# Kernel optimization log

Hardware: AMD Instinct MI355X
Metric: run time of the kernel (lower is better)

Reference implementation:

```python
import jax, jax.numpy as jnp
import numpy as np

N = 50000      # num nodes
E = 800000     # num edges (avg degree 16)
IN_FEA = 256
OU_FEA = 64


def setup_inputs() -> dict:
    key = jax.random.key(0)
    k_h, k_w, k_r, k_c, k_v = jax.random.split(key, 5)
    h = jax.random.normal(k_h, (N, IN_FEA), dtype=jnp.float32)
    # Linear(in_fea, ou_fea, bias=None): weight applied as h @ W, W [IN, OUT]
    W = jax.random.normal(k_w, (IN_FEA, OU_FEA), dtype=jnp.float32) / np.sqrt(IN_FEA)
    row = jax.random.randint(k_r, (E,), 0, N, dtype=jnp.int32)
    col = jax.random.randint(k_c, (E,), 0, N, dtype=jnp.int32)
    vals = jax.random.uniform(k_v, (E,), dtype=jnp.float32)
    return {"h": h, "W": W, "row": row, "col": col, "vals": vals}


def reference(h, W, row, col, vals):
    # dense projection: [N, IN] @ [IN, OUT] -> [N, OUT]
    hp = h @ W
    # torch builds sparse tensor with indices [col, row], i.e. G = A^T,
    # so torch.sparse.mm(G, hp)[i] = sum over edges with col==i of vals * hp[row]
    msg = hp[row] * vals[:, None]                      # [E, OUT] gather + scale
    out = jax.ops.segment_sum(msg, col, num_segments=N)  # scatter-add to dest
    return out
```

## Files before the change

### kernel.cpp

```cpp
#include <hip/hip_runtime.h>
#include <hip/hip_bf16.h>

#define IN_F 256
#define OU_F 64
#define BKN 128
#define BSHIFT 7
#define NBMAX 512
#define CHUNK 4096
#define STAGE_CAP 4096

typedef __attribute__((ext_vector_type(8))) short short8;
typedef __attribute__((ext_vector_type(4))) float f32x4;

__global__ void __launch_bounds__(256)
gemm_mfma_kernel(const float* __restrict__ h, const float* __restrict__ W,
                 __hip_bfloat16* __restrict__ hp, int* __restrict__ bcnt, int N)
{
    __shared__ unsigned short Wt[64][264];
    __shared__ uint4 hsv[2048];
    unsigned char* hs = reinterpret_cast<unsigned char*>(hsv);
    const int t = threadIdx.x;

    if (blockIdx.x == 0)
        for (int i = t; i <= NBMAX; i += 256) bcnt[i] = 0;

#pragma unroll
    for (int i = 0; i < 32; ++i) {
        int p  = t + i * 256;
        int c  = p & 63;
        int k0 = (p >> 6) << 1;
        float x = W[(size_t)k0 * OU_F + c];
        float y = W[(size_t)(k0 + 1) * OU_F + c];
        __hip_bfloat162 bb = __float22bfloat162_rn(make_float2(x, y));
        *reinterpret_cast<unsigned*>(&Wt[c][k0]) = *reinterpret_cast<unsigned*>(&bb);
    }

    const int rbase = blockIdx.x * 64;
    const int nrow  = min(64, N - rbase);
#pragma unroll
    for (int i = 0; i < 16; ++i) {
        int idx = t + i * 256;
        int r  = idx >> 6;
        int k4 = idx & 63;
        float4 v = make_float4(0.f, 0.f, 0.f, 0.f);
        if (r < nrow)
            v = reinterpret_cast<const float4*>(h)[(size_t)(rbase + r) * (IN_F / 4) + k4];
        __hip_bfloat162 lo = __float22bfloat162_rn(make_float2(v.x, v.y));
        __hip_bfloat162 hi = __float22bfloat162_rn(make_float2(v.z, v.w));
        unsigned boff = (unsigned)r * 512u + (((unsigned)k4 * 8u) ^ (((unsigned)r & 7u) << 4));
        uint2 pk;
        pk.x = *reinterpret_cast<unsigned*>(&lo);
        pk.y = *reinterpret_cast<unsigned*>(&hi);
        *reinterpret_cast<uint2*>(&hs[boff]) = pk;
    }
    __syncthreads();

    const int l    = t & 63;
    const int wv   = t >> 6;
    const int cl   = l & 15;
    const int kg   = l >> 4;
    const int rloc = wv * 16 + cl;

    f32x4 acc[4];
#pragma unroll
    for (int nt = 0; nt < 4; ++nt) acc[nt] = (f32x4){0.f, 0.f, 0.f, 0.f};

#pragma unroll
    for (int ks = 0; ks < 8; ++ks) {
        unsigned aoff = (unsigned)rloc * 512u +
                        (((unsigned)(ks * 64 + kg * 16)) ^ (((unsigned)rloc & 7u) << 4));
        short8 af = *reinterpret_cast<const short8*>(&hs[aoff]);
#pragma unroll
        for (int nt = 0; nt < 4; ++nt) {
            short8 bf = *reinterpret_cast<const short8*>(&Wt[nt * 16 + cl][ks * 32 + kg * 8]);
            acc[nt] = __builtin_amdgcn_mfma_f32_16x16x32_bf16(af, bf, acc[nt], 0, 0, 0);
        }
    }

#pragma unroll
    for (int nt = 0; nt < 4; ++nt)
#pragma unroll
        for (int rg = 0; rg < 4; ++rg) {
            int rr = rbase + wv * 16 + kg * 4 + rg;
            if (rr < N)
                hp[(size_t)rr * OU_F + nt * 16 + cl] = __float2bfloat16(acc[nt][rg]);
        }
}

__global__ void __launch_bounds__(256)
hist_scan_kernel(const int* __restrict__ col, int* __restrict__ bcnt,
                 int* __restrict__ boffs, int* __restrict__ bcursor, int E, int NB)
{
    __shared__ int lh[NBMAX];
    __shared__ int s[256];
    __shared__ int isLast;
    const int t = threadIdx.x;

    for (int i = t; i < NB; i += 256) lh[i] = 0;
    __syncthreads();

    const int n4 = E >> 2;
    const int4* c4 = (const int4*)col;
    for (int i = blockIdx.x * 256 + t; i < n4; i += gridDim.x * 256) {
        int4 v = c4[i];
        atomicAdd(&lh[v.x >> BSHIFT], 1);
        atomicAdd(&lh[v.y >> BSHIFT], 1);
        atomicAdd(&lh[v.z >> BSHIFT], 1);
        atomicAdd(&lh[v.w >> BSHIFT], 1);
    }
    if (blockIdx.x == 0)
        for (int e = (n4 << 2) + t; e < E; e += 256)
            atomicAdd(&lh[col[e] >> BSHIFT], 1);
    __syncthreads();

    for (int i = t; i < NB; i += 256)
        if (lh[i]) atomicAdd(&bcnt[i], lh[i]);

    __threadfence();
    if (t == 0) {
        int v = atomicAdd(&bcnt[NBMAX], 1);
        isLast = (v == (int)gridDim.x - 1);
    }
    __syncthreads();
    if (!isLast) return;

    for (int i = t; i < NB; i += 256)
        lh[i] = __hip_atomic_load(&bcnt[i], __ATOMIC_RELAXED, __HIP_MEMORY_SCOPE_AGENT);
    __syncthreads();

    int idx = t * 2;
    int c0 = (idx     < NB) ? lh[idx]     : 0;
    int c1 = (idx + 1 < NB) ? lh[idx + 1] : 0;
    int s0 = c0, s1 = s0 + c1;
    s[t] = s1;
    __syncthreads();
    for (int d = 1; d < 256; d <<= 1) {
        int v = (t >= d) ? s[t - d] : 0;
        __syncthreads();
        s[t] += v;
        __syncthreads();
    }
    int excl = (t > 0) ? s[t - 1] : 0;
    if (idx     < NB) { boffs[idx]     = excl;      bcursor[idx]     = excl;      }
    if (idx + 1 < NB) { boffs[idx + 1] = excl + s0; bcursor[idx + 1] = excl + s0; }
    if (t == 255) boffs[NB] = s[255];
}

__global__ void __launch_bounds__(256)
partition_kernel(const int* __restrict__ row, const int* __restrict__ col,
                 const float* __restrict__ vals, int* __restrict__ bcursor,
                 int2* __restrict__ epk, int E, int NB)
{
    __shared__ int  hist[NBMAX];
    __shared__ int  X[NBMAX];
    __shared__ int  gshift[NBMAX];
    __shared__ int  s[256];
    __shared__ int2 stage[CHUNK];
    __shared__ int  gpos[CHUNK];

    const int t = threadIdx.x;
    const int base = blockIdx.x * CHUNK;
    const int n = min(CHUNK, E - base);

    for (int i = t; i < NBMAX; i += 256) hist[i] = 0;
    __syncthreads();

#pragma unroll
    for (int k = 0; k < CHUNK / 256; ++k) {
        int i = t + k * 256;
        if (i < n) atomicAdd(&hist[col[base + i] >> BSHIFT], 1);
    }
    __syncthreads();

    int idx = t * 2;
    int c0 = hist[idx], c1 = hist[idx + 1];
    int s0 = c0, s1 = s0 + c1;
    s[t] = s1;
    __syncthreads();
    for (int d = 1; d < 256; d <<= 1) {
        int v = (t >= d) ? s[t - d] : 0;
        __syncthreads();
        s[t] += v;
        __syncthreads();
    }
    int excl = (t > 0) ? s[t - 1] : 0;
    X[idx]     = excl;
    X[idx + 1] = excl + s0;
    __syncthreads();

    for (int i = t; i < NB; i += 256) {
        int hcnt = hist[i];
        int g = hcnt ? atomicAdd(&bcursor[i], hcnt) : 0;
        gshift[i] = g - X[i];
    }
    __syncthreads();

#pragma unroll
    for (int k = 0; k < CHUNK / 256; ++k) {
        int i = t + k * 256;
        if (i < n) {
            int e  = base + i;
            int cv = col[e];
            int b  = cv >> BSHIFT;
            int r  = atomicAdd(&X[b], 1);
            unsigned pk = (unsigned)row[e] | ((unsigned)(cv & (BKN - 1)) << 17);
            stage[r] = make_int2((int)pk, __float_as_int(vals[e]));
            gpos[r]  = gshift[b] + r;
        }
    }
    __syncthreads();

#pragma unroll
    for (int k = 0; k < CHUNK / 256; ++k) {
        int i = t + k * 256;
        if (i < n) epk[gpos[i]] = stage[i];
    }
}

__global__ void __launch_bounds__(256)
csr_kernel(const int2* __restrict__ epk, const int* __restrict__ boffs,
           int2* __restrict__ epk2, int* __restrict__ node_offs,
           int N, int NB)
{
    __shared__ int  cnt[BKN];
    __shared__ int  sc[BKN];
    __shared__ int  cur[BKN];
    __shared__ int2 stage[STAGE_CAP];
    const int t = threadIdx.x;
    const int b = blockIdx.x;
    const int s = boffs[b], e = boffs[b + 1];
    const int n = e - s;
    const int node0 = b << BSHIFT;

    if (t < BKN) cnt[t] = 0;
    __syncthreads();
    for (int i = t; i < n; i += 256)
        atomicAdd(&cnt[((unsigned)epk[s + i].x) >> 17], 1);
    __syncthreads();

    if (t < BKN) sc[t] = cnt[t];
    __syncthreads();
    for (int d = 1; d < BKN; d <<= 1) {
        int v = 0;
        if (t < BKN && t >= d) v = sc[t - d];
        __syncthreads();
        if (t < BKN) sc[t] += v;
        __syncthreads();
    }
    if (t < BKN) {
        int excl = sc[t] - cnt[t];
        cur[t] = excl;
        int node = node0 + t;
        if (node < N) node_offs[node] = s + excl;
    }
    if (b == NB - 1 && t == 0) node_offs[N] = e;
    __syncthreads();

    if (n <= STAGE_CAP) {
        for (int i = t; i < n; i += 256) {
            int2 r = epk[s + i];
            int pos = atomicAdd(&cur[((unsigned)r.x) >> 17], 1);
            stage[pos] = r;
        }
        __syncthreads();
        for (int i = t; i < n; i += 256)
            epk2[s + i] = stage[i];
    } else {
        for (int i = t; i < n; i += 256) {
            int2 r = epk[s + i];
            int pos = atomicAdd(&cur[((unsigned)r.x) >> 17], 1);
            epk2[s + pos] = r;
        }
    }
}

__global__ void __launch_bounds__(256)
gather_kernel(const __hip_bfloat16* __restrict__ hp, const int* __restrict__ node_offs,
              const int2* __restrict__ epk2, float* __restrict__ out, int N)
{
    int wid  = (int)((blockIdx.x * 256u + threadIdx.x) >> 6);
    int lane = threadIdx.x & 63;
    if (wid >= N) return;
    int s = node_offs[wid], e = node_offs[wid + 1];
    float acc = 0.f;
    for (int base = s; base < e; base += 64) {
        int n = min(64, e - base);
        int2 m = make_int2(0, 0);
        if (lane < n) m = epk2[base + lane];
        int j = 0;
        for (; j + 4 <= n; j += 4) {
            unsigned r0 = (unsigned)__shfl(m.x, j)     & 0x1FFFFu;
            unsigned r1 = (unsigned)__shfl(m.x, j + 1) & 0x1FFFFu;
            unsigned r2 = (unsigned)__shfl(m.x, j + 2) & 0x1FFFFu;
            unsigned r3 = (unsigned)__shfl(m.x, j + 3) & 0x1FFFFu;
            float v0 = __int_as_float(__shfl(m.y, j));
            float v1 = __int_as_float(__shfl(m.y, j + 1));
            float v2 = __int_as_float(__shfl(m.y, j + 2));
            float v3 = __int_as_float(__shfl(m.y, j + 3));
            float x0 = __bfloat162float(hp[((size_t)r0 << 6) + lane]);
            float x1 = __bfloat162float(hp[((size_t)r1 << 6) + lane]);
            float x2 = __bfloat162float(hp[((size_t)r2 << 6) + lane]);
            float x3 = __bfloat162float(hp[((size_t)r3 << 6) + lane]);
            acc = fmaf(v0, x0, acc);
            acc = fmaf(v1, x1, acc);
            acc = fmaf(v2, x2, acc);
            acc = fmaf(v3, x3, acc);
        }
        for (; j < n; ++j) {
            unsigned r = (unsigned)__shfl(m.x, j) & 0x1FFFFu;
            float    v = __int_as_float(__shfl(m.y, j));
            acc = fmaf(v, __bfloat162float(hp[((size_t)r << 6) + lane]), acc);
        }
    }
    out[(size_t)wid * OU_F + lane] = acc;
}

__global__ void __launch_bounds__(256)
scatter_kernel(const __hip_bfloat16* __restrict__ hp, const int* __restrict__ row,
               const int* __restrict__ col, const float* __restrict__ vals,
               float* __restrict__ out, int E)
{
    unsigned int gid = blockIdx.x * 256u + threadIdx.x;
    int e = (int)(gid >> 6);
    if (e >= E) return;
    int f = (int)(gid & 63u);
    int r = row[e], c = col[e];
    float m = vals[e] * __bfloat162float(hp[(size_t)r * OU_F + f]);
    __hip_atomic_fetch_add(&out[(size_t)c * OU_F + f], m,
                           __ATOMIC_RELAXED, __HIP_MEMORY_SCOPE_AGENT);
}

extern "C" void kernel_launch(void* const* d_in, const int* in_sizes, int n_in,
                              void* d_out, int out_size, void* d_ws, size_t ws_size,
                              hipStream_t stream)
{
    const float* h    = (const float*)d_in[0];
    const float* W    = (const float*)d_in[1];
    const int*   row  = (const int*)d_in[2];
    const int*   col  = (const int*)d_in[3];
    const float* vals = (const float*)d_in[4];
    float*       out  = (float*)d_out;

    const int N = in_sizes[0] / IN_F;
    const int E = in_sizes[2];
    const int NB = (N + BKN - 1) / BKN;

    char*  ws  = (char*)d_ws;
    size_t off = 0;
    auto alloc = [&](size_t bytes) -> char* {
        char* p = ws + off;
        off = (off + bytes + 255) & ~(size_t)255;
        return p;
    };
    __hip_bfloat16* hp = (__hip_bfloat16*)alloc((size_t)N * OU_F * 2);
    int*   bcnt      = (int*)  alloc((size_t)(NBMAX + 1) * 4);
    int*   boffs     = (int*)  alloc((size_t)(NBMAX + 1) * 4);
    int*   bcursor   = (int*)  alloc((size_t)NBMAX * 4);
    int*   node_offs = (int*)  alloc((size_t)(N + 1) * 4);
    int2*  epk       = (int2*) alloc((size_t)E * 8);
    int2*  epk2      = (int2*) alloc((size_t)E * 8);
    const bool fits = (off <= ws_size) && (NB <= NBMAX) && (N < 131072);

    const int ntiles = (N + 63) / 64;
    gemm_mfma_kernel<<<ntiles, 256, 0, stream>>>(h, W, hp, bcnt, N);

    if (fits) {
        hist_scan_kernel<<<256, 256, 0, stream>>>(col, bcnt, boffs, bcursor, E, NB);
        partition_kernel<<<(E + CHUNK - 1) / CHUNK, 256, 0, stream>>>(
            row, col, vals, bcursor, epk, E, NB);
        csr_kernel<<<NB, 256, 0, stream>>>(epk, boffs, epk2, node_offs, N, NB);
        gather_kernel<<<(N + 3) / 4, 256, 0, stream>>>(hp, node_offs, epk2, out, N);
    } else {
        hipMemsetAsync(d_out, 0, (size_t)out_size * sizeof(float), stream);
        unsigned long long total = (unsigned long long)E * 64ull;
        unsigned int sgrid = (unsigned int)((total + 255ull) / 256ull);
        scatter_kernel<<<sgrid, 256, 0, stream>>>(hp, row, col, vals, out, E);
    }
}
```

Baseline: 95.52 us.

## Make GEMM persistent with register-resident W and direct global A loads

The projection GEMM becomes a persistent kernel: 512 blocks of 512 threads loop over 64-row tiles. The bf16 W is converted into shared memory once per block and then kept in registers as MFMA B fragments. Each wave now covers a 16-row by 32-column slice. The h rows are loaded straight from global memory into registers and converted to bf16, with no shared-memory staging or barrier per tile. This removes the per-tile W reconversion and the LDS round trip for A, but it raises register pressure and relies on uncoalesced per-lane row loads that are read by two column-group waves.

```diff
diff --git a/kernel.cpp b/kernel.cpp
--- a/kernel.cpp
+++ b/kernel.cpp
@@ -12,21 +12,30 @@
 typedef __attribute__((ext_vector_type(8))) short short8;
 typedef __attribute__((ext_vector_type(4))) float f32x4;
 
-__global__ void __launch_bounds__(256)
+__device__ inline short8 cvt8(float4 a, float4 b)
+{
+    union { short8 s8; __hip_bfloat162 h2[4]; } u;
+    u.h2[0] = __float22bfloat162_rn(make_float2(a.x, a.y));
+    u.h2[1] = __float22bfloat162_rn(make_float2(a.z, a.w));
+    u.h2[2] = __float22bfloat162_rn(make_float2(b.x, b.y));
+    u.h2[3] = __float22bfloat162_rn(make_float2(b.z, b.w));
+    return u.s8;
+}
+
+__global__ void __launch_bounds__(512, 4)
 gemm_mfma_kernel(const float* __restrict__ h, const float* __restrict__ W,
-                 __hip_bfloat16* __restrict__ hp, int* __restrict__ bcnt, int N)
+                 __hip_bfloat16* __restrict__ hp, int* __restrict__ bcnt,
+                 int N, int ntiles)
 {
     __shared__ unsigned short Wt[64][264];
-    __shared__ uint4 hsv[2048];
-    unsigned char* hs = reinterpret_cast<unsigned char*>(hsv);
     const int t = threadIdx.x;
 
     if (blockIdx.x == 0)
-        for (int i = t; i <= NBMAX; i += 256) bcnt[i] = 0;
-
-#pragma unroll
-    for (int i = 0; i < 32; ++i) {
-        int p  = t + i * 256;
+        for (int i = t; i <= NBMAX; i += 512) bcnt[i] = 0;
+
+#pragma unroll
+    for (int i = 0; i < 16; ++i) {
+        int p  = t + i * 512;
         int c  = p & 63;
         int k0 = (p >> 6) << 1;
         float x = W[(size_t)k0 * OU_F + c];
@@ -34,57 +43,50 @@
         __hip_bfloat162 bb = __float22bfloat162_rn(make_float2(x, y));
         *reinterpret_cast<unsigned*>(&Wt[c][k0]) = *reinterpret_cast<unsigned*>(&bb);
     }
-
-    const int rbase = blockIdx.x * 64;
-    const int nrow  = min(64, N - rbase);
-#pragma unroll
-    for (int i = 0; i < 16; ++i) {
-        int idx = t + i * 256;
-        int r  = idx >> 6;
-        int k4 = idx & 63;
-        float4 v = make_float4(0.f, 0.f, 0.f, 0.f);
-        if (r < nrow)
-            v = reinterpret_cast<const float4*>(h)[(size_t)(rbase + r) * (IN_F / 4) + k4];
-        __hip_bfloat162 lo = __float22bfloat162_rn(make_float2(v.x, v.y));
-        __hip_bfloat162 hi = __float22bfloat162_rn(make_float2(v.z, v.w));
-        unsigned boff = (unsigned)r * 512u + (((unsigned)k4 * 8u) ^ (((unsigned)r & 7u) << 4));
-        uint2 pk;
-        pk.x = *reinterpret_cast<unsigned*>(&lo);
-        pk.y = *reinterpret_cast<unsigned*>(&hi);
-        *reinterpret_cast<uint2*>(&hs[boff]) = pk;
-    }
-    __syncthreads();
-
-    const int l    = t & 63;
-    const int wv   = t >> 6;
-    const int cl   = l & 15;
-    const int kg   = l >> 4;
-    const int rloc = wv * 16 + cl;
-
-    f32x4 acc[4];
-#pragma unroll
-    for (int nt = 0; nt < 4; ++nt) acc[nt] = (f32x4){0.f, 0.f, 0.f, 0.f};
-
-#pragma unroll
-    for (int ks = 0; ks < 8; ++ks) {
-        unsigned aoff = (unsigned)rloc * 512u +
-                        (((unsigned)(ks * 64 + kg * 16)) ^ (((unsigned)rloc & 7u) << 4));
-        short8 af = *reinterpret_cast<const short8*>(&hs[aoff]);
-#pragma unroll
-        for (int nt = 0; nt < 4; ++nt) {
-            short8 bf = *reinterpret_cast<const short8*>(&Wt[nt * 16 + cl][ks * 32 + kg * 8]);
-            acc[nt] = __builtin_amdgcn_mfma_f32_16x16x32_bf16(af, bf, acc[nt], 0, 0, 0);
-        }
-    }
-
-#pragma unroll
-    for (int nt = 0; nt < 4; ++nt)
+    __syncthreads();
+
+    const int l   = t & 63;
+    const int wv  = t >> 6;
+    const int cl  = l & 15;
+    const int kg  = l >> 4;
+    const int rg4 = wv & 3;
+    const int cg  = wv >> 2;
+
+    short8 bfr[2][8];
+#pragma unroll
+    for (int nt2 = 0; nt2 < 2; ++nt2)
+#pragma unroll
+        for (int ks = 0; ks < 8; ++ks)
+            bfr[nt2][ks] = *reinterpret_cast<const short8*>(
+                &Wt[cg * 32 + nt2 * 16 + cl][ks * 32 + kg * 8]);
+
+    for (int tile = blockIdx.x; tile < ntiles; tile += gridDim.x) {
+        const int rbase = tile * 64 + rg4 * 16;
+        const int r     = rbase + cl;
+        const int rld   = min(r, N - 1);
+        const float4* hrow = reinterpret_cast<const float4*>(h) + (size_t)rld * (IN_F / 4);
+
+        f32x4 acc0 = (f32x4){0.f, 0.f, 0.f, 0.f};
+        f32x4 acc1 = (f32x4){0.f, 0.f, 0.f, 0.f};
+#pragma unroll
+        for (int ks = 0; ks < 8; ++ks) {
+            float4 a0 = hrow[ks * 8 + kg * 2];
+            float4 a1 = hrow[ks * 8 + kg * 2 + 1];
+            short8 af = cvt8(a0, a1);
+            acc0 = __builtin_amdgcn_mfma_f32_16x16x32_bf16(af, bfr[0][ks], acc0, 0, 0, 0);
+            acc1 = __builtin_amdgcn_mfma_f32_16x16x32_bf16(af, bfr[1][ks], acc1, 0, 0, 0);
+        }
+
 #pragma unroll
         for (int rg = 0; rg < 4; ++rg) {
-            int rr = rbase + wv * 16 + kg * 4 + rg;
-            if (rr < N)
-                hp[(size_t)rr * OU_F + nt * 16 + cl] = __float2bfloat16(acc[nt][rg]);
-        }
+            int rr = rbase + kg * 4 + rg;
+            if (rr < N) {
+                size_t base = (size_t)rr * OU_F + cg * 32 + cl;
+                hp[base]      = __float2bfloat16(acc0[rg]);
+                hp[base + 16] = __float2bfloat16(acc1[rg]);
+            }
+        }
+    }
 }
 
 __global__ void __launch_bounds__(256)
@@ -362,7 +364,7 @@
     const bool fits = (off <= ws_size) && (NB <= NBMAX) && (N < 131072);
 
     const int ntiles = (N + 63) / 64;
-    gemm_mfma_kernel<<<ntiles, 256, 0, stream>>>(h, W, hp, bcnt, N);
+    gemm_mfma_kernel<<<512, 512, 0, stream>>>(h, W, hp, bcnt, N, ntiles);
 
     if (fits) {
         hist_scan_kernel<<<256, 256, 0, stream>>>(col, bcnt, boffs, bcursor, E, NB);
```

New measurement: 94.50 us. Within noise of the previous version (-1.1%).
